# Kernel tuning notes

Measured on AMD Instinct MI355X. Metric: run time of the kernel, lower is better.

## Reference

```python
import jax, jax.numpy as jnp
import numpy as np

B, N, IN_DIM, OUT_DIM, HEADS = 4, 2048, 128, 32, 8
NEG_SLOPE = 0.2


def setup_inputs() -> dict:
    key = jax.random.key(0)
    k_x, k_adj, k_w, k_as, k_ad = jax.random.split(key, 5)
    x = jax.random.normal(k_x, (B, N, IN_DIM), dtype=jnp.float32)
    adj = jax.random.randint(k_adj, (B, N, N), 0, 2).astype(jnp.float32)
    # xavier_uniform bounds
    lim_w = float(np.sqrt(6.0 / (IN_DIM + OUT_DIM)))
    lim_a = float(np.sqrt(6.0 / (OUT_DIM + 1)))
    W = jax.random.uniform(k_w, (HEADS, IN_DIM, OUT_DIM), dtype=jnp.float32, minval=-lim_w, maxval=lim_w)
    a_src = jax.random.uniform(k_as, (HEADS, OUT_DIM), dtype=jnp.float32, minval=-lim_a, maxval=lim_a)
    a_dst = jax.random.uniform(k_ad, (HEADS, OUT_DIM), dtype=jnp.float32, minval=-lim_a, maxval=lim_a)
    return {"x": x, "adj": adj, "W": W, "a_src": a_src, "a_dst": a_dst}


def reference(x, adj, W, a_src, a_dst):
    # Wh: [B,H,N,O]
    Wh = jnp.einsum('bnf,hfo->bhno', x, W)
    alpha_src = jnp.einsum('bhno,ho->bhn', Wh, a_src)  # [B,H,N]
    alpha_dst = jnp.einsum('bhno,ho->bhn', Wh, a_dst)  # [B,H,N]
    # additive scores e[b,h,i,j] = alpha_src[b,h,i] + alpha_dst[b,h,j]
    e = alpha_src[..., :, None] + alpha_dst[..., None, :]
    e = jnp.where(e >= 0, e, NEG_SLOPE * e)  # leaky_relu(0.2)
    n = adj.shape[-1]
    eye = jnp.eye(n, dtype=adj.dtype)
    mask = (adj + eye[None] > 0)[:, None, :, :]  # [B,1,N,N]
    e = jnp.where(mask, e, -jnp.inf)
    attn = jax.nn.softmax(e, axis=-1)  # every row has self-loop -> finite
    out = jnp.einsum('bhij,bhjo->bhio', attn, Wh)  # [B,H,N,O]
    b = x.shape[0]
    out = jnp.transpose(out, (0, 2, 1, 3)).reshape(b, n, HEADS * OUT_DIM)
    return jax.nn.relu(out)
```

## Files before the change

kernel.cpp:

```cpp
#include <hip/hip_runtime.h>
#include <math.h>

#define BB 4
#define NSZ 2048
#define FDIM 128
#define ODIM 32
#define HH 8

typedef short short8 __attribute__((ext_vector_type(8)));
typedef float f32x4 __attribute__((ext_vector_type(4)));
typedef float f32x2 __attribute__((ext_vector_type(2)));

#define WS_EAP  0
#define WS_EBP  131072
#define WS_ADJB 262144
#define WS_WHF  786432

__device__ __forceinline__ unsigned bfbits(float f) {
    unsigned u = __builtin_bit_cast(unsigned, f);
    return u + 0x7fffu + ((u >> 16) & 1u);
}
__device__ __forceinline__ unsigned bfpack(float a, float b) {
    return __builtin_amdgcn_perm(bfbits(b), bfbits(a), 0x07060302);
}

__global__ __launch_bounds__(256) void k_prep(const float* __restrict__ x,
                                              const float* __restrict__ adj,
                                              const float* __restrict__ W,
                                              const float* __restrict__ a_src,
                                              const float* __restrict__ a_dst,
                                              unsigned* __restrict__ adjb,
                                              int4* __restrict__ whf,
                                              float2* __restrict__ eap,
                                              float2* __restrict__ ebp) {
    __shared__ float wsl[FDIM * 33];
    __shared__ unsigned short wlds[64][33];
    int t = threadIdx.x;

    if (blockIdx.x < 16384) {
        int g = blockIdx.x * 256 + t;
        int l = g & 7;
        int word = g >> 3;
        int wk = word & 63;
        int row = word >> 6;
        int i = row & (NSZ - 1);
        const float4 v = *(const float4*)&adj[(size_t)row * NSZ + wk * 32 + l * 4];
        unsigned m = 0;
        if (v.x > 0.f) m |= 1u << (l * 4 + 0);
        if (v.y > 0.f) m |= 1u << (l * 4 + 1);
        if (v.z > 0.f) m |= 1u << (l * 4 + 2);
        if (v.w > 0.f) m |= 1u << (l * 4 + 3);
        m |= (unsigned)__shfl_xor((int)m, 1);
        m |= (unsigned)__shfl_xor((int)m, 2);
        m |= (unsigned)__shfl_xor((int)m, 4);
        if (l == 0) {
            int jb = i - wk * 32;
            if (jb >= 0 && jb < 32) m |= 1u << jb;
            adjb[word] = m;
        }
        return;
    }

    int bidx = blockIdx.x - 16384;
    int b = bidx >> 8;
    int h = (bidx >> 5) & 7;
    int nt = bidx & 31;
    int n0 = nt * 64;
    int w = t >> 6, lane = t & 63;
    int col = lane & 15, quad = lane >> 4;

#pragma unroll
    for (int m = 0; m < 16; m++) {
        int idx = t + m * 256;
        wsl[(idx >> 5) * 33 + (idx & 31)] = W[(size_t)h * (FDIM * ODIM) + idx];
    }

    const float* xp = x + ((size_t)(b * NSZ) + n0 + w * 16 + col) * FDIM + quad * 8;
    int4 afr[4];
#pragma unroll
    for (int kt = 0; kt < 4; kt++) {
        float4 xa = *(const float4*)(xp + kt * 32);
        float4 xb = *(const float4*)(xp + kt * 32 + 4);
        afr[kt] = make_int4((int)bfpack(xa.x, xa.y), (int)bfpack(xa.z, xa.w),
                            (int)bfpack(xb.x, xb.y), (int)bfpack(xb.z, xb.w));
    }
    __syncthreads();

    f32x4 alo = {0.f, 0.f, 0.f, 0.f};
    f32x4 ahi = {0.f, 0.f, 0.f, 0.f};
#pragma unroll
    for (int kt = 0; kt < 4; kt++) {
        short8 a8 = __builtin_bit_cast(short8, afr[kt]);
#pragma unroll
        for (int ot = 0; ot < 2; ot++) {
            unsigned d[4];
#pragma unroll
            for (int jp = 0; jp < 4; jp++) {
                float lo = wsl[(kt * 32 + quad * 8 + 2 * jp) * 33 + ot * 16 + col];
                float hi = wsl[(kt * 32 + quad * 8 + 2 * jp + 1) * 33 + ot * 16 + col];
                d[jp] = bfpack(lo, hi);
            }
            int4 bf = make_int4((int)d[0], (int)d[1], (int)d[2], (int)d[3]);
            if (ot == 0)
                alo = __builtin_amdgcn_mfma_f32_16x16x32_bf16(a8,
                        __builtin_bit_cast(short8, bf), alo, 0, 0, 0);
            else
                ahi = __builtin_amdgcn_mfma_f32_16x16x32_bf16(a8,
                        __builtin_bit_cast(short8, bf), ahi, 0, 0, 0);
        }
    }

    float as0 = a_src[h * ODIM + col], as1 = a_src[h * ODIM + 16 + col];
    float ad0 = a_dst[h * ODIM + col], ad1 = a_dst[h * ODIM + 16 + col];
#pragma unroll
    for (int r = 0; r < 4; r++) {
        float pa = alo[r] * as0 + ahi[r] * as1;
        float pb = alo[r] * ad0 + ahi[r] * ad1;
#pragma unroll
        for (int mk = 1; mk <= 8; mk <<= 1) {
            pa += __shfl_xor(pa, mk);
            pb += __shfl_xor(pb, mk);
        }
        if (col == 0) {
            size_t idx = (size_t)(b * HH + h) * NSZ + n0 + w * 16 + quad * 4 + r;
            eap[idx] = make_float2(__expf(pa - 8.f), __expf(0.2f * pa - 8.f));
            ebp[idx] = make_float2(__expf(pb - 8.f), __expf(0.2f * pb - 8.f));
        }
    }

#pragma unroll
    for (int r = 0; r < 4; r++) {
        wlds[w * 16 + quad * 4 + r][col]      = (unsigned short)(bfbits(alo[r]) >> 16);
        wlds[w * 16 + quad * 4 + r][col + 16] = (unsigned short)(bfbits(ahi[r]) >> 16);
    }
    __syncthreads();
    int jl = w >> 1, ot = w & 1;
    unsigned d[4];
#pragma unroll
    for (int jp = 0; jp < 4; jp++) {
        unsigned lo = wlds[jl * 32 + quad * 8 + 2 * jp][ot * 16 + col];
        unsigned hi = wlds[jl * 32 + quad * 8 + 2 * jp + 1][ot * 16 + col];
        d[jp] = (hi << 16) | lo;
    }
    int fragid = ((b * HH + h) * 64 + nt * 2 + jl) * 2 + ot;
    whf[(size_t)fragid * 64 + lane] = make_int4((int)d[0], (int)d[1], (int)d[2], (int)d[3]);
}

__device__ __forceinline__ int4 pfrag(f32x2 ea, const f32x4& l0,
                                      const f32x4& l1, const f32x4& l2,
                                      const f32x4& l3, unsigned w,
                                      const unsigned (*__restrict__ mlut)[2]) {
    f32x2 r0 = __builtin_shufflevector(l0, l0, 0, 1) * ea;
    f32x2 r1 = __builtin_shufflevector(l0, l0, 2, 3) * ea;
    f32x2 r2 = __builtin_shufflevector(l1, l1, 0, 1) * ea;
    f32x2 r3 = __builtin_shufflevector(l1, l1, 2, 3) * ea;
    f32x2 r4 = __builtin_shufflevector(l2, l2, 0, 1) * ea;
    f32x2 r5 = __builtin_shufflevector(l2, l2, 2, 3) * ea;
    f32x2 r6 = __builtin_shufflevector(l3, l3, 0, 1) * ea;
    f32x2 r7 = __builtin_shufflevector(l3, l3, 2, 3) * ea;
    float p0 = fmaxf(r0.x, r0.y);
    float p1 = fmaxf(r1.x, r1.y);
    float p2 = fmaxf(r2.x, r2.y);
    float p3 = fmaxf(r3.x, r3.y);
    float p4 = fmaxf(r4.x, r4.y);
    float p5 = fmaxf(r5.x, r5.y);
    float p6 = fmaxf(r6.x, r6.y);
    float p7 = fmaxf(r7.x, r7.y);
    unsigned d0, d1, d2, d3;
    asm("v_cvt_pk_bf16_f32 %0, %1, %2" : "=v"(d0) : "v"(p0), "v"(p1));
    asm("v_cvt_pk_bf16_f32 %0, %1, %2" : "=v"(d1) : "v"(p2), "v"(p3));
    asm("v_cvt_pk_bf16_f32 %0, %1, %2" : "=v"(d2) : "v"(p4), "v"(p5));
    asm("v_cvt_pk_bf16_f32 %0, %1, %2" : "=v"(d3) : "v"(p6), "v"(p7));
    const unsigned* mA = mlut[w & 15];
    const unsigned* mB = mlut[(w >> 4) & 15];
    return make_int4((int)(d0 & mA[0]), (int)(d1 & mA[1]),
                     (int)(d2 & mB[0]), (int)(d3 & mB[1]));
}

__global__ __launch_bounds__(256) void k_gat(const int4* __restrict__ whf,
                                             const float2* __restrict__ eap,
                                             const float2* __restrict__ ebp,
                                             const unsigned* __restrict__ adjb,
                                             float* __restrict__ out) {
    __shared__ float ebl[4096];
    __shared__ float comb[2][24][64];
    __shared__ unsigned mlut[16][2];

    int t = threadIdx.x;
    int u = blockIdx.x;
    int unit = (u & 7) * 128 + (u >> 3);
    int b = unit >> 8;
    int h = (unit >> 5) & 7;
    int i0 = (unit & 31) * 64;
    int wave = t >> 6, lane = t & 63;
    int it = wave & 1, jh = wave >> 1;
    int col = lane & 15, quad = lane >> 4, qsh = quad * 8;
    size_t bh = (size_t)(b * HH + h);

    if (t < 16) {
        mlut[t][0] = ((t & 1) ? 0x0000FFFFu : 0u) | ((t & 2) ? 0xFFFF0000u : 0u);
        mlut[t][1] = ((t & 4) ? 0x0000FFFFu : 0u) | ((t & 8) ? 0xFFFF0000u : 0u);
    }

    const float4* ebg = (const float4*)(ebp + bh * NSZ);
#pragma unroll
    for (int k = 0; k < 4; k++) ((float4*)ebl)[t + k * 256] = ebg[t + k * 256];

    int iw = i0 + it * 32;
    float2 ea0 = eap[bh * NSZ + iw + col];
    float2 ea1 = eap[bh * NSZ + iw + 16 + col];
    f32x2 ea0v = {ea0.x, ea0.y};
    f32x2 ea1v = {ea1.x, ea1.y};
    const uint4* mp0 = (const uint4*)(adjb + ((size_t)(b * NSZ) + iw + col) * 64) + jh * 8;
    const uint4* mp1 = (const uint4*)(adjb + ((size_t)(b * NSZ) + iw + 16 + col) * 64) + jh * 8;
    const int4* bfp = whf + bh * 8192 + lane;

    f32x4 a00 = {0.f,0.f,0.f,0.f}, a01 = {0.f,0.f,0.f,0.f}, a0d = {0.f,0.f,0.f,0.f};
    f32x4 a10 = {0.f,0.f,0.f,0.f}, a11 = {0.f,0.f,0.f,0.f}, a1d = {0.f,0.f,0.f,0.f};
    const int4 onesv = make_int4(0x3F803F80, 0x3F803F80, 0x3F803F80, 0x3F803F80);
    short8 bones = __builtin_bit_cast(short8, onesv);

    __syncthreads();

    for (int jt4 = 0; jt4 < 8; jt4++) {
        uint4 m0 = mp0[jt4];
        uint4 m1 = mp1[jt4];
        unsigned m0a[4] = {m0.x, m0.y, m0.z, m0.w};
        unsigned m1a[4] = {m1.x, m1.y, m1.z, m1.w};
#pragma unroll
        for (int q = 0; q < 4; q++) {
            int jt = jh * 32 + jt4 * 4 + q;
            const f32x4* el = (const f32x4*)&ebl[(jt * 32 + qsh) * 2];
            f32x4 l0 = el[0], l1 = el[1], l2 = el[2], l3 = el[3];
            int4 blo = bfp[jt * 128];
            int4 bhi = bfp[jt * 128 + 64];
            int4 f0 = pfrag(ea0v, l0, l1, l2, l3, m0a[q] >> qsh, mlut);
            int4 f1 = pfrag(ea1v, l0, l1, l2, l3, m1a[q] >> qsh, mlut);
            short8 af0 = __builtin_bit_cast(short8, f0);
            short8 af1 = __builtin_bit_cast(short8, f1);
            short8 b0 = __builtin_bit_cast(short8, blo);
            short8 b1 = __builtin_bit_cast(short8, bhi);
            a00 = __builtin_amdgcn_mfma_f32_16x16x32_bf16(af0, b0, a00, 0, 0, 0);
            a01 = __builtin_amdgcn_mfma_f32_16x16x32_bf16(af0, b1, a01, 0, 0, 0);
            a0d = __builtin_amdgcn_mfma_f32_16x16x32_bf16(af0, bones, a0d, 0, 0, 0);
            a10 = __builtin_amdgcn_mfma_f32_16x16x32_bf16(af1, b0, a10, 0, 0, 0);
            a11 = __builtin_amdgcn_mfma_f32_16x16x32_bf16(af1, b1, a11, 0, 0, 0);
            a1d = __builtin_amdgcn_mfma_f32_16x16x32_bf16(af1, bones, a1d, 0, 0, 0);
        }
    }

    if (jh) {
#pragma unroll
        for (int r = 0; r < 4; r++) {
            comb[it][r][lane]      = a00[r];
            comb[it][4 + r][lane]  = a01[r];
            comb[it][8 + r][lane]  = a0d[r];
            comb[it][12 + r][lane] = a10[r];
            comb[it][16 + r][lane] = a11[r];
            comb[it][20 + r][lane] = a1d[r];
        }
    }
    __syncthreads();
    if (jh) return;
#pragma unroll
    for (int r = 0; r < 4; r++) {
        a00[r] += comb[it][r][lane];
        a01[r] += comb[it][4 + r][lane];
        a0d[r] += comb[it][8 + r][lane];
        a10[r] += comb[it][12 + r][lane];
        a11[r] += comb[it][16 + r][lane];
        a1d[r] += comb[it][20 + r][lane];
    }

    float* op = out + ((size_t)(b * NSZ) + iw) * (HH * ODIM) + h * ODIM + col;
#pragma unroll
    for (int r = 0; r < 4; r++) {
        int row = quad * 4 + r;
        float inv0 = 1.0f / a0d[r];
        float inv1 = 1.0f / a1d[r];
        op[(size_t)row * (HH * ODIM)]           = fmaxf(a00[r] * inv0, 0.f);
        op[(size_t)row * (HH * ODIM) + 16]      = fmaxf(a01[r] * inv0, 0.f);
        op[(size_t)(row + 16) * (HH * ODIM)]      = fmaxf(a10[r] * inv1, 0.f);
        op[(size_t)(row + 16) * (HH * ODIM) + 16] = fmaxf(a11[r] * inv1, 0.f);
    }
}

extern "C" void kernel_launch(void* const* d_in, const int* in_sizes, int n_in,
                              void* d_out, int out_size, void* d_ws, size_t ws_size,
                              hipStream_t stream) {
    const float* x     = (const float*)d_in[0];
    const float* adj   = (const float*)d_in[1];
    const float* W     = (const float*)d_in[2];
    const float* a_src = (const float*)d_in[3];
    const float* a_dst = (const float*)d_in[4];
    float* out = (float*)d_out;

    float* ws = (float*)d_ws;
    float2* eap    = (float2*)(ws + WS_EAP);
    float2* ebp    = (float2*)(ws + WS_EBP);
    unsigned* adjb = (unsigned*)(ws + WS_ADJB);
    int4* whf      = (int4*)(ws + WS_WHF);

    k_prep<<<dim3(16384 + 1024), dim3(256), 0, stream>>>(x, adj, W, a_src, a_dst,
                                                         adjb, whf, eap, ebp);
    k_gat<<<dim3(BB * HH * (NSZ / 64)), dim3(256), 0, stream>>>(whf, eap, ebp, adjb, out);
}
```

Before: 136.7 us.

## Split j across four waves, reuse B fragments over four row tiles

Each wave now covers all 64 rows of the block (four 16-row tiles) over a quarter of the j range, where before it covered 32 rows over half. Each loaded Wh B-fragment and e_b vector therefore feeds four A-fragments instead of two. The probability fragment is also reworked: the leaky-relu max pairs a structure-of-arrays e_b/e_b^0.2 layout with the two e_a factors, and the mask expansion uses bfe/bfi instructions in place of a shared-memory LUT. The cost is more accumulator registers (launch bounds of 4 blocks per CU are set) and a two-stage shared-memory reduction across four waves.

```diff
diff --git a/kernel.cpp b/kernel.cpp
--- a/kernel.cpp
+++ b/kernel.cpp
@@ -32,7 +32,8 @@
                                               unsigned* __restrict__ adjb,
                                               int4* __restrict__ whf,
                                               float2* __restrict__ eap,
-                                              float2* __restrict__ ebp) {
+                                              float* __restrict__ ebe,
+                                              float* __restrict__ ebe2) {
     __shared__ float wsl[FDIM * 33];
     __shared__ unsigned short wlds[64][33];
     int t = threadIdx.x;
@@ -124,7 +125,8 @@
         if (col == 0) {
             size_t idx = (size_t)(b * HH + h) * NSZ + n0 + w * 16 + quad * 4 + r;
             eap[idx] = make_float2(__expf(pa - 8.f), __expf(0.2f * pa - 8.f));
-            ebp[idx] = make_float2(__expf(pb - 8.f), __expf(0.2f * pb - 8.f));
+            ebe[idx]  = __expf(pb - 8.f);
+            ebe2[idx] = __expf(0.2f * pb - 8.f);
         }
     }
 
@@ -146,45 +148,47 @@
     whf[(size_t)fragid * 64 + lane] = make_int4((int)d[0], (int)d[1], (int)d[2], (int)d[3]);
 }
 
-__device__ __forceinline__ int4 pfrag(f32x2 ea, const f32x4& l0,
-                                      const f32x4& l1, const f32x4& l2,
-                                      const f32x4& l3, unsigned w,
-                                      const unsigned (*__restrict__ mlut)[2]) {
-    f32x2 r0 = __builtin_shufflevector(l0, l0, 0, 1) * ea;
-    f32x2 r1 = __builtin_shufflevector(l0, l0, 2, 3) * ea;
-    f32x2 r2 = __builtin_shufflevector(l1, l1, 0, 1) * ea;
-    f32x2 r3 = __builtin_shufflevector(l1, l1, 2, 3) * ea;
-    f32x2 r4 = __builtin_shufflevector(l2, l2, 0, 1) * ea;
-    f32x2 r5 = __builtin_shufflevector(l2, l2, 2, 3) * ea;
-    f32x2 r6 = __builtin_shufflevector(l3, l3, 0, 1) * ea;
-    f32x2 r7 = __builtin_shufflevector(l3, l3, 2, 3) * ea;
-    float p0 = fmaxf(r0.x, r0.y);
-    float p1 = fmaxf(r1.x, r1.y);
-    float p2 = fmaxf(r2.x, r2.y);
-    float p3 = fmaxf(r3.x, r3.y);
-    float p4 = fmaxf(r4.x, r4.y);
-    float p5 = fmaxf(r5.x, r5.y);
-    float p6 = fmaxf(r6.x, r6.y);
-    float p7 = fmaxf(r7.x, r7.y);
+template<int B>
+__device__ __forceinline__ unsigned mexp2(unsigned w, unsigned selhi) {
+    unsigned lo, hi, r;
+    asm("v_bfe_i32 %0, %1, %2, 1" : "=v"(lo) : "v"(w), "i"(B));
+    asm("v_bfe_i32 %0, %1, %2, 1" : "=v"(hi) : "v"(w), "i"(B + 1));
+    asm("v_bfi_b32 %0, %1, %2, %3" : "=v"(r) : "s"(selhi), "v"(hi), "v"(lo));
+    return r;
+}
+
+__device__ __forceinline__ int4 pfrag(float eaa, float eab,
+                                      f32x4 e0, f32x4 e1, f32x4 g0, f32x4 g1,
+                                      unsigned w8, unsigned selhi) {
+    f32x2 ea2 = {eaa, eaa}, eb2 = {eab, eab};
+    f32x2 p0 = __builtin_elementwise_max(__builtin_shufflevector(e0, e0, 0, 1) * ea2,
+                                         __builtin_shufflevector(g0, g0, 0, 1) * eb2);
+    f32x2 p1 = __builtin_elementwise_max(__builtin_shufflevector(e0, e0, 2, 3) * ea2,
+                                         __builtin_shufflevector(g0, g0, 2, 3) * eb2);
+    f32x2 p2 = __builtin_elementwise_max(__builtin_shufflevector(e1, e1, 0, 1) * ea2,
+                                         __builtin_shufflevector(g1, g1, 0, 1) * eb2);
+    f32x2 p3 = __builtin_elementwise_max(__builtin_shufflevector(e1, e1, 2, 3) * ea2,
+                                         __builtin_shufflevector(g1, g1, 2, 3) * eb2);
     unsigned d0, d1, d2, d3;
-    asm("v_cvt_pk_bf16_f32 %0, %1, %2" : "=v"(d0) : "v"(p0), "v"(p1));
-    asm("v_cvt_pk_bf16_f32 %0, %1, %2" : "=v"(d1) : "v"(p2), "v"(p3));
-    asm("v_cvt_pk_bf16_f32 %0, %1, %2" : "=v"(d2) : "v"(p4), "v"(p5));
-    asm("v_cvt_pk_bf16_f32 %0, %1, %2" : "=v"(d3) : "v"(p6), "v"(p7));
-    const unsigned* mA = mlut[w & 15];
-    const unsigned* mB = mlut[(w >> 4) & 15];
-    return make_int4((int)(d0 & mA[0]), (int)(d1 & mA[1]),
-                     (int)(d2 & mB[0]), (int)(d3 & mB[1]));
-}
-
-__global__ __launch_bounds__(256) void k_gat(const int4* __restrict__ whf,
-                                             const float2* __restrict__ eap,
-                                             const float2* __restrict__ ebp,
-                                             const unsigned* __restrict__ adjb,
-                                             float* __restrict__ out) {
-    __shared__ float ebl[4096];
-    __shared__ float comb[2][24][64];
-    __shared__ unsigned mlut[16][2];
+    asm("v_cvt_pk_bf16_f32 %0, %1, %2" : "=v"(d0) : "v"(p0.x), "v"(p0.y));
+    asm("v_cvt_pk_bf16_f32 %0, %1, %2" : "=v"(d1) : "v"(p1.x), "v"(p1.y));
+    asm("v_cvt_pk_bf16_f32 %0, %1, %2" : "=v"(d2) : "v"(p2.x), "v"(p2.y));
+    asm("v_cvt_pk_bf16_f32 %0, %1, %2" : "=v"(d3) : "v"(p3.x), "v"(p3.y));
+    return make_int4((int)(d0 & mexp2<0>(w8, selhi)),
+                     (int)(d1 & mexp2<2>(w8, selhi)),
+                     (int)(d2 & mexp2<4>(w8, selhi)),
+                     (int)(d3 & mexp2<6>(w8, selhi)));
+}
+
+__global__ __launch_bounds__(256, 4) void k_gat(const int4* __restrict__ whf,
+                                                const float2* __restrict__ eap,
+                                                const float* __restrict__ ebe,
+                                                const float* __restrict__ ebe2,
+                                                const unsigned* __restrict__ adjb,
+                                                float* __restrict__ out) {
+    __shared__ __align__(16) char smem[24576];
+    float* eble = (float*)smem;
+    float* eblf = (float*)(smem + 8192);
 
     int t = threadIdx.x;
     int u = blockIdx.x;
@@ -193,95 +197,119 @@
     int h = (unit >> 5) & 7;
     int i0 = (unit & 31) * 64;
     int wave = t >> 6, lane = t & 63;
-    int it = wave & 1, jh = wave >> 1;
     int col = lane & 15, quad = lane >> 4, qsh = quad * 8;
     size_t bh = (size_t)(b * HH + h);
-
-    if (t < 16) {
-        mlut[t][0] = ((t & 1) ? 0x0000FFFFu : 0u) | ((t & 2) ? 0xFFFF0000u : 0u);
-        mlut[t][1] = ((t & 4) ? 0x0000FFFFu : 0u) | ((t & 8) ? 0xFFFF0000u : 0u);
-    }
-
-    const float4* ebg = (const float4*)(ebp + bh * NSZ);
-#pragma unroll
-    for (int k = 0; k < 4; k++) ((float4*)ebl)[t + k * 256] = ebg[t + k * 256];
-
-    int iw = i0 + it * 32;
-    float2 ea0 = eap[bh * NSZ + iw + col];
-    float2 ea1 = eap[bh * NSZ + iw + 16 + col];
-    f32x2 ea0v = {ea0.x, ea0.y};
-    f32x2 ea1v = {ea1.x, ea1.y};
-    const uint4* mp0 = (const uint4*)(adjb + ((size_t)(b * NSZ) + iw + col) * 64) + jh * 8;
-    const uint4* mp1 = (const uint4*)(adjb + ((size_t)(b * NSZ) + iw + 16 + col) * 64) + jh * 8;
+    const unsigned selhi = 0xFFFF0000u;
+
+    const float4* ege = (const float4*)(ebe + bh * NSZ);
+    const float4* egf = (const float4*)(ebe2 + bh * NSZ);
+    ((float4*)eble)[t]       = ege[t];
+    ((float4*)eble)[t + 256] = ege[t + 256];
+    ((float4*)eblf)[t]       = egf[t];
+    ((float4*)eblf)[t + 256] = egf[t + 256];
+
+    float eaa[4], eab[4];
+#pragma unroll
+    for (int tt = 0; tt < 4; tt++) {
+        float2 ev = eap[bh * NSZ + i0 + tt * 16 + col];
+        eaa[tt] = ev.x;
+        eab[tt] = ev.y;
+    }
+    const char* mbase = (const char*)(adjb + ((size_t)(b * NSZ) + i0 + col) * 64)
+                        + (size_t)wave * 64;
     const int4* bfp = whf + bh * 8192 + lane;
 
-    f32x4 a00 = {0.f,0.f,0.f,0.f}, a01 = {0.f,0.f,0.f,0.f}, a0d = {0.f,0.f,0.f,0.f};
-    f32x4 a10 = {0.f,0.f,0.f,0.f}, a11 = {0.f,0.f,0.f,0.f}, a1d = {0.f,0.f,0.f,0.f};
+    f32x4 acc[4][2], accd[4];
+#pragma unroll
+    for (int tt = 0; tt < 4; tt++) {
+        acc[tt][0] = (f32x4){0.f, 0.f, 0.f, 0.f};
+        acc[tt][1] = (f32x4){0.f, 0.f, 0.f, 0.f};
+        accd[tt]   = (f32x4){0.f, 0.f, 0.f, 0.f};
+    }
     const int4 onesv = make_int4(0x3F803F80, 0x3F803F80, 0x3F803F80, 0x3F803F80);
     short8 bones = __builtin_bit_cast(short8, onesv);
 
     __syncthreads();
 
-    for (int jt4 = 0; jt4 < 8; jt4++) {
-        uint4 m0 = mp0[jt4];
-        uint4 m1 = mp1[jt4];
-        unsigned m0a[4] = {m0.x, m0.y, m0.z, m0.w};
-        unsigned m1a[4] = {m1.x, m1.y, m1.z, m1.w};
+    for (int jt4 = 0; jt4 < 4; jt4++) {
+        uint4 m0 = *(const uint4*)(mbase + 0 * 4096 + jt4 * 16);
+        uint4 m1 = *(const uint4*)(mbase + 1 * 4096 + jt4 * 16);
+        uint4 m2 = *(const uint4*)(mbase + 2 * 4096 + jt4 * 16);
+        uint4 m3 = *(const uint4*)(mbase + 3 * 4096 + jt4 * 16);
+        unsigned ma[4][4] = {{m0.x, m0.y, m0.z, m0.w},
+                             {m1.x, m1.y, m1.z, m1.w},
+                             {m2.x, m2.y, m2.z, m2.w},
+                             {m3.x, m3.y, m3.z, m3.w}};
 #pragma unroll
         for (int q = 0; q < 4; q++) {
-            int jt = jh * 32 + jt4 * 4 + q;
-            const f32x4* el = (const f32x4*)&ebl[(jt * 32 + qsh) * 2];
-            f32x4 l0 = el[0], l1 = el[1], l2 = el[2], l3 = el[3];
+            int jt = wave * 16 + jt4 * 4 + q;
+            const f32x4* pe = (const f32x4*)&eble[jt * 32 + qsh];
+            const f32x4* pf = (const f32x4*)&eblf[jt * 32 + qsh];
+            f32x4 e0 = pe[0], e1 = pe[1];
+            f32x4 g0 = pf[0], g1 = pf[1];
             int4 blo = bfp[jt * 128];
             int4 bhi = bfp[jt * 128 + 64];
-            int4 f0 = pfrag(ea0v, l0, l1, l2, l3, m0a[q] >> qsh, mlut);
-            int4 f1 = pfrag(ea1v, l0, l1, l2, l3, m1a[q] >> qsh, mlut);
-            short8 af0 = __builtin_bit_cast(short8, f0);
-            short8 af1 = __builtin_bit_cast(short8, f1);
             short8 b0 = __builtin_bit_cast(short8, blo);
             short8 b1 = __builtin_bit_cast(short8, bhi);
-            a00 = __builtin_amdgcn_mfma_f32_16x16x32_bf16(af0, b0, a00, 0, 0, 0);
-            a01 = __builtin_amdgcn_mfma_f32_16x16x32_bf16(af0, b1, a01, 0, 0, 0);
-            a0d = __builtin_amdgcn_mfma_f32_16x16x32_bf16(af0, bones, a0d, 0, 0, 0);
-            a10 = __builtin_amdgcn_mfma_f32_16x16x32_bf16(af1, b0, a10, 0, 0, 0);
-            a11 = __builtin_amdgcn_mfma_f32_16x16x32_bf16(af1, b1, a11, 0, 0, 0);
-            a1d = __builtin_amdgcn_mfma_f32_16x16x32_bf16(af1, bones, a1d, 0, 0, 0);
-        }
-    }
-
-    if (jh) {
+#pragma unroll
+            for (int tt = 0; tt < 4; tt++) {
+                int4 fr = pfrag(eaa[tt], eab[tt], e0, e1, g0, g1,
+                                ma[tt][q] >> qsh, selhi);
+                short8 af = __builtin_bit_cast(short8, fr);
+                acc[tt][0] = __builtin_amdgcn_mfma_f32_16x16x32_bf16(af, b0, acc[tt][0], 0, 0, 0);
+                acc[tt][1] = __builtin_amdgcn_mfma_f32_16x16x32_bf16(af, b1, acc[tt][1], 0, 0, 0);
+                accd[tt]   = __builtin_amdgcn_mfma_f32_16x16x32_bf16(af, bones, accd[tt], 0, 0, 0);
+            }
+        }
+    }
+
+    f32x4 (*cb)[12][64] = (f32x4 (*)[12][64])smem;
+    __syncthreads();
+    if (wave >= 2) {
+#pragma unroll
+        for (int tt = 0; tt < 4; tt++) {
+            cb[wave - 2][tt * 3 + 0][lane] = acc[tt][0];
+            cb[wave - 2][tt * 3 + 1][lane] = acc[tt][1];
+            cb[wave - 2][tt * 3 + 2][lane] = accd[tt];
+        }
+    }
+    __syncthreads();
+    if (wave < 2) {
+#pragma unroll
+        for (int tt = 0; tt < 4; tt++) {
+            acc[tt][0] += cb[wave][tt * 3 + 0][lane];
+            acc[tt][1] += cb[wave][tt * 3 + 1][lane];
+            accd[tt]   += cb[wave][tt * 3 + 2][lane];
+        }
+    }
+    __syncthreads();
+    if (wave == 1) {
+#pragma unroll
+        for (int tt = 0; tt < 4; tt++) {
+            cb[0][tt * 3 + 0][lane] = acc[tt][0];
+            cb[0][tt * 3 + 1][lane] = acc[tt][1];
+            cb[0][tt * 3 + 2][lane] = accd[tt];
+        }
+    }
+    __syncthreads();
+    if (wave != 0) return;
+#pragma unroll
+    for (int tt = 0; tt < 4; tt++) {
+        acc[tt][0] += cb[0][tt * 3 + 0][lane];
+        acc[tt][1] += cb[0][tt * 3 + 1][lane];
+        accd[tt]   += cb[0][tt * 3 + 2][lane];
+    }
+
+    float* op = out + ((size_t)(b * NSZ) + i0) * (HH * ODIM) + h * ODIM + col;
+#pragma unroll
+    for (int tt = 0; tt < 4; tt++) {
 #pragma unroll
         for (int r = 0; r < 4; r++) {
-            comb[it][r][lane]      = a00[r];
-            comb[it][4 + r][lane]  = a01[r];
-            comb[it][8 + r][lane]  = a0d[r];
-            comb[it][12 + r][lane] = a10[r];
-            comb[it][16 + r][lane] = a11[r];
-            comb[it][20 + r][lane] = a1d[r];
-        }
-    }
-    __syncthreads();
-    if (jh) return;
-#pragma unroll
-    for (int r = 0; r < 4; r++) {
-        a00[r] += comb[it][r][lane];
-        a01[r] += comb[it][4 + r][lane];
-        a0d[r] += comb[it][8 + r][lane];
-        a10[r] += comb[it][12 + r][lane];
-        a11[r] += comb[it][16 + r][lane];
-        a1d[r] += comb[it][20 + r][lane];
-    }
-
-    float* op = out + ((size_t)(b * NSZ) + iw) * (HH * ODIM) + h * ODIM + col;
-#pragma unroll
-    for (int r = 0; r < 4; r++) {
-        int row = quad * 4 + r;
-        float inv0 = 1.0f / a0d[r];
-        float inv1 = 1.0f / a1d[r];
-        op[(size_t)row * (HH * ODIM)]           = fmaxf(a00[r] * inv0, 0.f);
-        op[(size_t)row * (HH * ODIM) + 16]      = fmaxf(a01[r] * inv0, 0.f);
-        op[(size_t)(row + 16) * (HH * ODIM)]      = fmaxf(a10[r] * inv1, 0.f);
-        op[(size_t)(row + 16) * (HH * ODIM) + 16] = fmaxf(a11[r] * inv1, 0.f);
+            int row = tt * 16 + quad * 4 + r;
+            float inv = 1.0f / accd[tt][r];
+            op[(size_t)row * (HH * ODIM)]      = fmaxf(acc[tt][0][r] * inv, 0.f);
+            op[(size_t)row * (HH * ODIM) + 16] = fmaxf(acc[tt][1][r] * inv, 0.f);
+        }
     }
 }
 
@@ -297,11 +325,12 @@
 
     float* ws = (float*)d_ws;
     float2* eap    = (float2*)(ws + WS_EAP);
-    float2* ebp    = (float2*)(ws + WS_EBP);
+    float* ebe     = ws + WS_EBP;
+    float* ebe2    = ws + WS_EBP + 65536;
     unsigned* adjb = (unsigned*)(ws + WS_ADJB);
     int4* whf      = (int4*)(ws + WS_WHF);
 
     k_prep<<<dim3(16384 + 1024), dim3(256), 0, stream>>>(x, adj, W, a_src, a_dst,
-                                                         adjb, whf, eap, ebp);
-    k_gat<<<dim3(BB * HH * (NSZ / 64)), dim3(256), 0, stream>>>(whf, eap, ebp, adjb, out);
-}
+                                                         adjb, whf, eap, ebe, ebe2);
+    k_gat<<<dim3(BB * HH * (NSZ / 64)), dim3(256), 0, stream>>>(whf, eap, ebe, ebe2, adjb, out);
+}
```

Result: slower. 152.6 us (+11.6%).
